# Performance work log

Measured on AMD Instinct MI355X. Metric: run time of the kernel, lower is better.

The kernel has to match this reference:

```python
import jax, jax.numpy as jnp
import numpy as np
import math

B, S, D = 8, 4096, 128  # batch, seq_len, embed_dim == attention_head_size
EPS = 1e-5


def layer_norm(x, w, b):
    mu = jnp.mean(x, axis=-1, keepdims=True)
    var = jnp.var(x, axis=-1, keepdims=True)
    return (x - mu) * jax.lax.rsqrt(var + EPS) * w + b


def setup_inputs() -> dict:
    key = jax.random.key(0)
    ks = jax.random.split(key, 4)
    x = jax.random.normal(ks[0], (B, S, D), dtype=jnp.float32)
    Wq = jax.random.normal(ks[1], (D, D), dtype=jnp.float32) / math.sqrt(D)
    Wk = jax.random.normal(ks[2], (D, D), dtype=jnp.float32) / math.sqrt(D)
    Wv = jax.random.normal(ks[3], (D, D), dtype=jnp.float32) / math.sqrt(D)
    qn_w = jnp.ones((D,), dtype=jnp.float32)
    qn_b = jnp.zeros((D,), dtype=jnp.float32)
    kn_w = jnp.ones((D,), dtype=jnp.float32)
    kn_b = jnp.zeros((D,), dtype=jnp.float32)
    return {"x": x, "Wq": Wq, "Wk": Wk, "Wv": Wv,
            "qn_w": qn_w, "qn_b": qn_b, "kn_w": kn_w, "kn_b": kn_b}


def reference(x, Wq, Wk, Wv, qn_w, qn_b, kn_w, kn_b):
    # q/k/v projections (nn.Linear with no bias: x @ W^T)
    q = layer_norm(jnp.einsum('bsd,hd->bsh', x, Wq), qn_w, qn_b)
    k = layer_norm(jnp.einsum('bsd,hd->bsh', x, Wk), kn_w, kn_b)
    v = jnp.einsum('bsd,hd->bsh', x, Wv)
    scale = math.sqrt(D)
    scores = jnp.einsum('bqh,bkh->bqk', q, k) / scale  # [B, S, S]
    attn = jax.nn.softmax(scores, axis=-1)
    # dropout_rate = 0.0 -> identity
    return jnp.einsum('bqk,bkh->bqh', attn, v)
```

## Files before the change

### kernel.cpp

```cpp
#include <hip/hip_runtime.h>

#define B_ 8
#define S_ 4096
#define D_ 128
#define KVB 64
#define NT (S_ / KVB)

typedef __attribute__((ext_vector_type(4))) float f32x4;
typedef __attribute__((ext_vector_type(16))) float f32x16;
typedef __attribute__((ext_vector_type(8))) short s16x8;

__device__ __forceinline__ unsigned short f2bf(float f) {
    union { float f; unsigned u; } v; v.f = f;
    unsigned r = (v.u + 0x7fffu + ((v.u >> 16) & 1u)) >> 16;
    return (unsigned short)r;
}

__device__ __forceinline__ unsigned cvt_pk(float lo, float hi) {
    unsigned r;
    asm("v_cvt_pk_bf16_f32 %0, %1, %2" : "=v"(r) : "v"(lo), "v"(hi));
    return r;
}

__device__ __forceinline__ s16x8 load_cvt8(const float* p) {
    f32x4 a = *(const f32x4*)p;
    f32x4 b = *(const f32x4*)(p + 4);
    s16x8 r;
    r[0] = (short)f2bf(a[0]); r[1] = (short)f2bf(a[1]);
    r[2] = (short)f2bf(a[2]); r[3] = (short)f2bf(a[3]);
    r[4] = (short)f2bf(b[0]); r[5] = (short)f2bf(b[1]);
    r[6] = (short)f2bf(b[2]); r[7] = (short)f2bf(b[3]);
    return r;
}

__device__ __forceinline__ void gld16(unsigned short* lds, const unsigned short* g) {
    __builtin_amdgcn_global_load_lds(
        (const __attribute__((address_space(1))) unsigned int*)g,
        (__attribute__((address_space(3))) unsigned int*)lds,
        16, 0, 0);
}

__global__ __launch_bounds__(256, 1) void proj_kernel(
    const float* __restrict__ x,  const float* __restrict__ Wq,
    const float* __restrict__ Wk, const float* __restrict__ Wv,
    const float* __restrict__ qn_w, const float* __restrict__ qn_b,
    const float* __restrict__ kn_w, const float* __restrict__ kn_b,
    unsigned short* __restrict__ qo, unsigned short* __restrict__ ko,
    unsigned short* __restrict__ vto)
{
    __shared__ unsigned short wlds[128 * 136];
    __shared__ unsigned short vstage[128 * 72];

    const int tid  = threadIdx.x;
    const int lane = tid & 63;
    const int wv   = tid >> 6;
    const int j    = lane & 15;
    const int g    = lane >> 4;

    const int b    = blockIdx.x >> 6;
    const int sblk = (blockIdx.x & 63) * 64;
    const int srow = sblk + wv * 16;

    const float* xrow = x + ((size_t)b * S_ + srow + j) * D_;
    s16x8 af[4];
#pragma unroll
    for (int kk = 0; kk < 4; ++kk) af[kk] = load_cvt8(xrow + kk * 32 + g * 8);

    const int wrow = tid >> 1;
    const int wcol = (tid & 1) * 64;

#pragma unroll 1
    for (int m = 0; m < 3; ++m) {
        const float* Wm = (m == 0) ? Wq : (m == 1) ? Wk : Wv;
        __syncthreads();
#pragma unroll
        for (int it = 0; it < 8; ++it) {
            int col = wcol + it * 8;
            *(s16x8*)&wlds[wrow * 136 + col] = load_cvt8(Wm + wrow * 128 + col);
        }
        __syncthreads();

        f32x4 acc[8];
#pragma unroll
        for (int ct = 0; ct < 8; ++ct) { f32x4 z = {0.f, 0.f, 0.f, 0.f}; acc[ct] = z; }
#pragma unroll
        for (int ct = 0; ct < 8; ++ct) {
#pragma unroll
            for (int kk = 0; kk < 4; ++kk) {
                s16x8 bf = *(const s16x8*)&wlds[(ct * 16 + j) * 136 + kk * 32 + g * 8];
                acc[ct] = __builtin_amdgcn_mfma_f32_16x16x32_bf16(af[kk], bf, acc[ct], 0, 0, 0);
            }
        }

        if (m < 2) {
            const float* lw = (m == 0) ? qn_w : kn_w;
            const float* lb = (m == 0) ? qn_b : kn_b;
            float sum[4], sq[4];
#pragma unroll
            for (int r = 0; r < 4; ++r) {
                float s1 = 0.f, s2 = 0.f;
#pragma unroll
                for (int ct = 0; ct < 8; ++ct) { float v = acc[ct][r]; s1 += v; s2 += v * v; }
#pragma unroll
                for (int msk = 1; msk < 16; msk <<= 1) {
                    s1 += __shfl_xor(s1, msk);
                    s2 += __shfl_xor(s2, msk);
                }
                sum[r] = s1; sq[r] = s2;
            }
            float gwv[8], gbv[8];
#pragma unroll
            for (int ct = 0; ct < 8; ++ct) { gwv[ct] = lw[ct * 16 + j]; gbv[ct] = lb[ct * 16 + j]; }
            unsigned short* dst = (m == 0) ? qo : ko;
            const float post = (m == 0) ? 0.12751742361888f : 1.0f;
#pragma unroll
            for (int r = 0; r < 4; ++r) {
                float mean = sum[r] * (1.f / 128.f);
                float var  = sq[r] * (1.f / 128.f) - mean * mean;
                float rstd = rsqrtf(var + 1e-5f);
                size_t rowoff = ((size_t)b * S_ + sblk + wv * 16 + g * 4 + r) * D_;
#pragma unroll
                for (int ct = 0; ct < 8; ++ct) {
                    float val = ((acc[ct][r] - mean) * rstd * gwv[ct] + gbv[ct]) * post;
                    dst[rowoff + ct * 16 + j] = f2bf(val);
                }
            }
        } else {
#pragma unroll
            for (int ct = 0; ct < 8; ++ct) {
#pragma unroll
                for (int r = 0; r < 4; ++r) {
                    vstage[(ct * 16 + j) * 72 + wv * 16 + g * 4 + r] = f2bf(acc[ct][r]);
                }
            }
            __syncthreads();
            int h  = tid >> 1;
            int cb = (tid & 1) * 32;
#pragma unroll
            for (int c = 0; c < 4; ++c) {
                *(s16x8*)(vto + ((size_t)b * D_ + h) * S_ + sblk + cb + c * 8) =
                    *(const s16x8*)&vstage[h * 72 + cb + c * 8];
            }
        }
    }
}

__global__ __launch_bounds__(256, 2) void attn_kernel(
    const unsigned short* __restrict__ qb, const unsigned short* __restrict__ kb,
    const unsigned short* __restrict__ vtb, float* __restrict__ out)
{
    __shared__ unsigned short kbuf[2][KVB * D_];
    __shared__ unsigned short vbuf[2][D_ * KVB];

    const int tid  = threadIdx.x;
    const int lane = tid & 63;
    const int wv   = tid >> 6;
    const int qg   = wv & 1;
    const int kh   = wv >> 1;
    const int a    = lane & 31;
    const int hh   = lane >> 5;

    const int blk = (a >> 2) & 3;
    const int pa  = (blk == 1) ? a + 4 : (blk == 2) ? a - 4 : a;

    const int swz = (blockIdx.x & 7) * 64 + (blockIdx.x >> 3);
    const int b   = swz >> 6;
    const int s0  = (swz & 63) * 64;

    const unsigned short* qptr = qb + ((size_t)b * S_ + s0 + qg * 32 + a) * D_;
    s16x8 qf[8];
#pragma unroll
    for (int kk = 0; kk < 8; ++kk) qf[kk] = *(const s16x8*)(qptr + kk * 16 + hh * 8);

    const unsigned short* kg_base = kb  + (size_t)b * S_ * D_;
    const unsigned short* vg_base = vtb + (size_t)b * D_ * S_;

    auto STAGE = [&](int bi, int kt2) {
        const int kv0 = kt2 * KVB;
#pragma unroll
        for (int it = 0; it < 4; ++it) {
            const int row = wv * 16 + it * 4 + (lane >> 4);
            const unsigned short* src =
                kg_base + (size_t)(kv0 + row) * D_ + (((lane & 15) ^ (row & 15)) << 3);
            gld16(&kbuf[bi][(wv * 16 + it * 4) * D_], src);
        }
#pragma unroll
        for (int it = 0; it < 4; ++it) {
            const int row = wv * 32 + it * 8 + (lane >> 3);
            const unsigned short* src =
                vg_base + (size_t)row * S_ + kv0 + (((lane & 7) ^ ((lane >> 3) & 7)) << 3);
            gld16(&vbuf[bi][(wv * 32 + it * 8) * KVB], src);
        }
    };

    STAGE(0, 0);
    STAGE(1, 1);

    f32x16 acc[4], ld;
#pragma unroll
    for (int dt = 0; dt < 4; ++dt)
#pragma unroll
        for (int e = 0; e < 16; ++e) acc[dt][e] = 0.f;
#pragma unroll
    for (int e = 0; e < 16; ++e) ld[e] = 0.f;

    s16x8 ones;
#pragma unroll
    for (int e = 0; e < 8; ++e) ones[e] = (short)0x3F80;

    const int kbase = (32 * kh + pa) * D_;
    const int kswz  = pa & 15;
    const int vswz  = lane & 7;

    s16x8 vfr[8];
    union PU { unsigned u[4]; s16x8 v; };
    PU P0, P1;

#pragma unroll 1
    for (int kt = 0; kt < NT; ++kt) {
        const int cur = kt & 1;
        if (kt + 1 < NT) { asm volatile("s_waitcnt vmcnt(8)" ::: "memory"); }
        else             { asm volatile("s_waitcnt vmcnt(0)" ::: "memory"); }
        __builtin_amdgcn_s_barrier();
        asm volatile("" ::: "memory");

        const unsigned short* kl = kbuf[cur];
        const unsigned short* vl = vbuf[cur];

        s16x8 kf[8];
#pragma unroll
        for (int kk = 0; kk < 8; ++kk)
            kf[kk] = *(const s16x8*)&kl[kbase + (((2 * kk + hh) ^ kswz) << 3)];

        if (kt) {
            __builtin_amdgcn_s_setprio(1);
            ld = __builtin_amdgcn_mfma_f32_32x32x16_bf16(P0.v, ones, ld, 0, 0, 0);
            ld = __builtin_amdgcn_mfma_f32_32x32x16_bf16(P1.v, ones, ld, 0, 0, 0);
            acc[0] = __builtin_amdgcn_mfma_f32_32x32x16_bf16(P0.v, vfr[0], acc[0], 0, 0, 0);
            acc[0] = __builtin_amdgcn_mfma_f32_32x32x16_bf16(P1.v, vfr[1], acc[0], 0, 0, 0);
            acc[1] = __builtin_amdgcn_mfma_f32_32x32x16_bf16(P0.v, vfr[2], acc[1], 0, 0, 0);
            acc[1] = __builtin_amdgcn_mfma_f32_32x32x16_bf16(P1.v, vfr[3], acc[1], 0, 0, 0);
            __builtin_amdgcn_s_setprio(0);
        }
#pragma unroll
        for (int dt = 0; dt < 2; ++dt)
#pragma unroll
            for (int km = 0; km < 2; ++km)
                vfr[dt * 2 + km] = *(const s16x8*)
                    &vl[(32 * dt + a) * KVB + (((4 * kh + 2 * km + hh) ^ vswz) << 3)];
        if (kt) {
            __builtin_amdgcn_s_setprio(1);
            acc[2] = __builtin_amdgcn_mfma_f32_32x32x16_bf16(P0.v, vfr[4], acc[2], 0, 0, 0);
            acc[2] = __builtin_amdgcn_mfma_f32_32x32x16_bf16(P1.v, vfr[5], acc[2], 0, 0, 0);
            acc[3] = __builtin_amdgcn_mfma_f32_32x32x16_bf16(P0.v, vfr[6], acc[3], 0, 0, 0);
            acc[3] = __builtin_amdgcn_mfma_f32_32x32x16_bf16(P1.v, vfr[7], acc[3], 0, 0, 0);
            __builtin_amdgcn_s_setprio(0);
        }
#pragma unroll
        for (int dt = 2; dt < 4; ++dt)
#pragma unroll
            for (int km = 0; km < 2; ++km)
                vfr[dt * 2 + km] = *(const s16x8*)
                    &vl[(32 * dt + a) * KVB + (((4 * kh + 2 * km + hh) ^ vswz) << 3)];

        asm volatile("s_waitcnt lgkmcnt(0)" ::: "memory");
        __builtin_amdgcn_s_barrier();
        asm volatile("" ::: "memory");

        if (kt + 2 < NT) STAGE(cur, kt + 2);

        f32x16 svA, svB;
#pragma unroll
        for (int e = 0; e < 16; ++e) { svA[e] = 0.f; svB[e] = 0.f; }
        __builtin_amdgcn_s_setprio(1);
#pragma unroll
        for (int kk = 0; kk < 4; ++kk) {
            svA = __builtin_amdgcn_mfma_f32_32x32x16_bf16(kf[kk],     qf[kk],     svA, 0, 0, 0);
            svB = __builtin_amdgcn_mfma_f32_32x32x16_bf16(kf[kk + 4], qf[kk + 4], svB, 0, 0, 0);
        }
        __builtin_amdgcn_s_setprio(0);

        float p[16];
#pragma unroll
        for (int e = 0; e < 16; ++e) p[e] = exp2f(svA[e] + svB[e]);
        P0.u[0] = cvt_pk(p[0],  p[1]);  P0.u[1] = cvt_pk(p[2],  p[3]);
        P0.u[2] = cvt_pk(p[4],  p[5]);  P0.u[3] = cvt_pk(p[6],  p[7]);
        P1.u[0] = cvt_pk(p[8],  p[9]);  P1.u[1] = cvt_pk(p[10], p[11]);
        P1.u[2] = cvt_pk(p[12], p[13]); P1.u[3] = cvt_pk(p[14], p[15]);
    }

    {
        __builtin_amdgcn_s_setprio(1);
        ld = __builtin_amdgcn_mfma_f32_32x32x16_bf16(P0.v, ones, ld, 0, 0, 0);
        ld = __builtin_amdgcn_mfma_f32_32x32x16_bf16(P1.v, ones, ld, 0, 0, 0);
#pragma unroll
        for (int dt = 0; dt < 4; ++dt) {
            acc[dt] = __builtin_amdgcn_mfma_f32_32x32x16_bf16(P0.v, vfr[dt * 2 + 0], acc[dt], 0, 0, 0);
            acc[dt] = __builtin_amdgcn_mfma_f32_32x32x16_bf16(P1.v, vfr[dt * 2 + 1], acc[dt], 0, 0, 0);
        }
        __builtin_amdgcn_s_setprio(0);
    }

    __syncthreads();

    float* csum = (float*)&kbuf[0][0];
    float* lsum = (float*)&vbuf[0][0];
    if (kh == 1) {
#pragma unroll
        for (int dt = 0; dt < 4; ++dt)
#pragma unroll
            for (int rr = 0; rr < 4; ++rr) {
                f32x4 c4 = { acc[dt][rr*4+0], acc[dt][rr*4+1], acc[dt][rr*4+2], acc[dt][rr*4+3] };
                *(f32x4*)&csum[((qg * 4 + dt) * 4 + rr) * 256 + lane * 4] = c4;
            }
#pragma unroll
        for (int rr = 0; rr < 4; ++rr) {
            f32x4 l4 = { ld[rr*4+0], ld[rr*4+1], ld[rr*4+2], ld[rr*4+3] };
            *(f32x4*)&lsum[(qg * 4 + rr) * 256 + lane * 4] = l4;
        }
    }
    __syncthreads();
    if (kh == 0) {
        float li[16];
#pragma unroll
        for (int rr = 0; rr < 4; ++rr) {
            f32x4 lt = *(const f32x4*)&lsum[(qg * 4 + rr) * 256 + lane * 4];
#pragma unroll
            for (int e = 0; e < 4; ++e) li[rr * 4 + e] = 1.0f / (ld[rr * 4 + e] + lt[e]);
        }
#pragma unroll
        for (int dt = 0; dt < 4; ++dt) {
#pragma unroll
            for (int rr = 0; rr < 4; ++rr) {
                f32x4 o4 = *(const f32x4*)&csum[((qg * 4 + dt) * 4 + rr) * 256 + lane * 4];
#pragma unroll
                for (int e = 0; e < 4; ++e) {
                    const int r = rr * 4 + e;
                    const int qrow = (r & 3) + 8 * (r >> 2) + 4 * hh;
                    out[((size_t)b * S_ + s0 + qg * 32 + qrow) * D_ + 32 * dt + a] =
                        (acc[dt][r] + o4[e]) * li[r];
                }
            }
        }
    }
}

extern "C" void kernel_launch(void* const* d_in, const int* in_sizes, int n_in,
                              void* d_out, int out_size, void* d_ws, size_t ws_size,
                              hipStream_t stream) {
    const float* x    = (const float*)d_in[0];
    const float* Wq   = (const float*)d_in[1];
    const float* Wk   = (const float*)d_in[2];
    const float* Wv   = (const float*)d_in[3];
    const float* qn_w = (const float*)d_in[4];
    const float* qn_b = (const float*)d_in[5];
    const float* kn_w = (const float*)d_in[6];
    const float* kn_b = (const float*)d_in[7];
    float* out = (float*)d_out;

    const size_t n = (size_t)B_ * S_ * D_;
    unsigned short* qws  = (unsigned short*)d_ws;
    unsigned short* kws  = qws + n;
    unsigned short* vtws = kws + n;

    proj_kernel<<<512, 256, 0, stream>>>(x, Wq, Wk, Wv, qn_w, qn_b, kn_w, kn_b,
                                         qws, kws, vtws);
    attn_kernel<<<512, 256, 0, stream>>>(qws, kws, vtws, out);
}
```

Before: 128.2 us.

## Use single-wave attention blocks with 32-row KV tiles and no barriers

Each attention workgroup shrinks from four waves sharing 64 query rows and a 64-key tile to one wave owning 32 query rows and a 32-key tile, launched as 1024 blocks. Because one wave now covers every KV column, the cross-wave reduction through shared memory and all block barriers go away, and the V staging swizzle is redone for the narrower tile. The costs are twice as many tile iterations, each with less MFMA work to hide global and LDS latency. K/V tiles also get less reuse per block, since each one is loaded for 32 query rows instead of 64, and the grid is only 1024 single-wave blocks to occupy the GPU.

```diff
diff --git a/kernel.cpp b/kernel.cpp
--- a/kernel.cpp
+++ b/kernel.cpp
@@ -3,7 +3,7 @@
 #define B_ 8
 #define S_ 4096
 #define D_ 128
-#define KVB 64
+#define KVB 32
 #define NT (S_ / KVB)
 
 typedef __attribute__((ext_vector_type(4))) float f32x4;
@@ -145,29 +145,25 @@
     }
 }
 
-__global__ __launch_bounds__(256, 2) void attn_kernel(
+__global__ __launch_bounds__(64) void attn_kernel(
     const unsigned short* __restrict__ qb, const unsigned short* __restrict__ kb,
     const unsigned short* __restrict__ vtb, float* __restrict__ out)
 {
     __shared__ unsigned short kbuf[2][KVB * D_];
     __shared__ unsigned short vbuf[2][D_ * KVB];
 
-    const int tid  = threadIdx.x;
-    const int lane = tid & 63;
-    const int wv   = tid >> 6;
-    const int qg   = wv & 1;
-    const int kh   = wv >> 1;
+    const int lane = threadIdx.x & 63;
     const int a    = lane & 31;
     const int hh   = lane >> 5;
 
     const int blk = (a >> 2) & 3;
     const int pa  = (blk == 1) ? a + 4 : (blk == 2) ? a - 4 : a;
 
-    const int swz = (blockIdx.x & 7) * 64 + (blockIdx.x >> 3);
-    const int b   = swz >> 6;
-    const int s0  = (swz & 63) * 64;
-
-    const unsigned short* qptr = qb + ((size_t)b * S_ + s0 + qg * 32 + a) * D_;
+    const int swz = (blockIdx.x & 7) * 128 + (blockIdx.x >> 3);
+    const int b   = swz >> 7;
+    const int s0  = (swz & 127) * 32;
+
+    const unsigned short* qptr = qb + ((size_t)b * S_ + s0 + a) * D_;
     s16x8 qf[8];
 #pragma unroll
     for (int kk = 0; kk < 8; ++kk) qf[kk] = *(const s16x8*)(qptr + kk * 16 + hh * 8);
@@ -178,18 +174,19 @@
     auto STAGE = [&](int bi, int kt2) {
         const int kv0 = kt2 * KVB;
 #pragma unroll
-        for (int it = 0; it < 4; ++it) {
-            const int row = wv * 16 + it * 4 + (lane >> 4);
+        for (int it = 0; it < 8; ++it) {
+            const int row = it * 4 + (lane >> 4);
             const unsigned short* src =
                 kg_base + (size_t)(kv0 + row) * D_ + (((lane & 15) ^ (row & 15)) << 3);
-            gld16(&kbuf[bi][(wv * 16 + it * 4) * D_], src);
-        }
-#pragma unroll
-        for (int it = 0; it < 4; ++it) {
-            const int row = wv * 32 + it * 8 + (lane >> 3);
+            gld16(&kbuf[bi][(it * 4) * D_], src);
+        }
+#pragma unroll
+        for (int it = 0; it < 8; ++it) {
+            const int row = it * 16 + (lane >> 2);
+            const int gg  = (row ^ (row >> 2)) & 3;
             const unsigned short* src =
-                vg_base + (size_t)row * S_ + kv0 + (((lane & 7) ^ ((lane >> 3) & 7)) << 3);
-            gld16(&vbuf[bi][(wv * 32 + it * 8) * KVB], src);
+                vg_base + (size_t)row * S_ + kv0 + (((lane & 3) ^ gg) << 3);
+            gld16(&vbuf[bi][(it * 16) * KVB], src);
         }
     };
 
@@ -208,9 +205,9 @@
 #pragma unroll
     for (int e = 0; e < 8; ++e) ones[e] = (short)0x3F80;
 
-    const int kbase = (32 * kh + pa) * D_;
+    const int kbase = pa * D_;
     const int kswz  = pa & 15;
-    const int vswz  = lane & 7;
+    const int vswz  = (a ^ (a >> 2)) & 3;
 
     s16x8 vfr[8];
     union PU { unsigned u[4]; s16x8 v; };
@@ -219,10 +216,8 @@
 #pragma unroll 1
     for (int kt = 0; kt < NT; ++kt) {
         const int cur = kt & 1;
-        if (kt + 1 < NT) { asm volatile("s_waitcnt vmcnt(8)" ::: "memory"); }
-        else             { asm volatile("s_waitcnt vmcnt(0)" ::: "memory"); }
-        __builtin_amdgcn_s_barrier();
-        asm volatile("" ::: "memory");
+        if (kt + 1 < NT) { asm volatile("s_waitcnt vmcnt(16)" ::: "memory"); }
+        else             { asm volatile("s_waitcnt vmcnt(0)"  ::: "memory"); }
 
         const unsigned short* kl = kbuf[cur];
         const unsigned short* vl = vbuf[cur];
@@ -247,7 +242,7 @@
 #pragma unroll
             for (int km = 0; km < 2; ++km)
                 vfr[dt * 2 + km] = *(const s16x8*)
-                    &vl[(32 * dt + a) * KVB + (((4 * kh + 2 * km + hh) ^ vswz) << 3)];
+                    &vbuf[cur][(32 * dt + a) * KVB + (((2 * km + hh) ^ vswz) << 3)];
         if (kt) {
             __builtin_amdgcn_s_setprio(1);
             acc[2] = __builtin_amdgcn_mfma_f32_32x32x16_bf16(P0.v, vfr[4], acc[2], 0, 0, 0);
@@ -261,12 +256,9 @@
 #pragma unroll
             for (int km = 0; km < 2; ++km)
                 vfr[dt * 2 + km] = *(const s16x8*)
-                    &vl[(32 * dt + a) * KVB + (((4 * kh + 2 * km + hh) ^ vswz) << 3)];
+                    &vl[(32 * dt + a) * KVB + (((2 * km + hh) ^ vswz) << 3)];
 
         asm volatile("s_waitcnt lgkmcnt(0)" ::: "memory");
-        __builtin_amdgcn_s_barrier();
-        asm volatile("" ::: "memory");
-
         if (kt + 2 < NT) STAGE(cur, kt + 2);
 
         f32x16 svA, svB;
@@ -301,46 +293,15 @@
         __builtin_amdgcn_s_setprio(0);
     }
 
-    __syncthreads();
-
-    float* csum = (float*)&kbuf[0][0];
-    float* lsum = (float*)&vbuf[0][0];
-    if (kh == 1) {
-#pragma unroll
-        for (int dt = 0; dt < 4; ++dt)
-#pragma unroll
-            for (int rr = 0; rr < 4; ++rr) {
-                f32x4 c4 = { acc[dt][rr*4+0], acc[dt][rr*4+1], acc[dt][rr*4+2], acc[dt][rr*4+3] };
-                *(f32x4*)&csum[((qg * 4 + dt) * 4 + rr) * 256 + lane * 4] = c4;
-            }
-#pragma unroll
-        for (int rr = 0; rr < 4; ++rr) {
-            f32x4 l4 = { ld[rr*4+0], ld[rr*4+1], ld[rr*4+2], ld[rr*4+3] };
-            *(f32x4*)&lsum[(qg * 4 + rr) * 256 + lane * 4] = l4;
-        }
-    }
-    __syncthreads();
-    if (kh == 0) {
-        float li[16];
-#pragma unroll
-        for (int rr = 0; rr < 4; ++rr) {
-            f32x4 lt = *(const f32x4*)&lsum[(qg * 4 + rr) * 256 + lane * 4];
-#pragma unroll
-            for (int e = 0; e < 4; ++e) li[rr * 4 + e] = 1.0f / (ld[rr * 4 + e] + lt[e]);
-        }
-#pragma unroll
-        for (int dt = 0; dt < 4; ++dt) {
-#pragma unroll
-            for (int rr = 0; rr < 4; ++rr) {
-                f32x4 o4 = *(const f32x4*)&csum[((qg * 4 + dt) * 4 + rr) * 256 + lane * 4];
-#pragma unroll
-                for (int e = 0; e < 4; ++e) {
-                    const int r = rr * 4 + e;
-                    const int qrow = (r & 3) + 8 * (r >> 2) + 4 * hh;
-                    out[((size_t)b * S_ + s0 + qg * 32 + qrow) * D_ + 32 * dt + a] =
-                        (acc[dt][r] + o4[e]) * li[r];
-                }
-            }
+    float li[16];
+#pragma unroll
+    for (int r = 0; r < 16; ++r) li[r] = 1.0f / ld[r];
+#pragma unroll
+    for (int dt = 0; dt < 4; ++dt) {
+#pragma unroll
+        for (int r = 0; r < 16; ++r) {
+            const int qrow = (r & 3) + 8 * (r >> 2) + 4 * hh;
+            out[((size_t)b * S_ + s0 + qrow) * D_ + 32 * dt + a] = acc[dt][r] * li[r];
         }
     }
 }
@@ -365,5 +326,5 @@
 
     proj_kernel<<<512, 256, 0, stream>>>(x, Wq, Wk, Wv, qn_w, qn_b, kn_w, kn_b,
                                          qws, kws, vtws);
-    attn_kernel<<<512, 256, 0, stream>>>(qws, kws, vtws, out);
-}
+    attn_kernel<<<1024, 64, 0, stream>>>(qws, kws, vtws, out);
+}
```

Result: slower. 153.8 us (+20.0%).
